# Kernel tuning notes

Hardware: AMD Instinct MI355X
Metric: run time of the kernel (lower is better)

## Reference

```python
import jax, jax.numpy as jnp
import numpy as np
from jax import lax

NUM_TAGS = 126
T = NUM_TAGS + 2          # tag_size = 128
B, S = 256, 512
START, STOP = T - 3, T - 2
NEG = -10000.0


def setup_inputs() -> dict:
    key = jax.random.key(0)
    k1, k2, k3 = jax.random.split(key, 3)
    feats = jax.random.normal(k1, (B, S, T), jnp.float32)
    # learned transition matrix with the module's init masking pattern
    trans = jax.random.normal(k2, (T, T), jnp.float32)
    trans = trans.at[:, START].set(NEG).at[STOP, :].set(NEG)
    trans = trans.at[:, 0].set(NEG).at[0, :].set(NEG)
    # prefix masks with varying valid lengths in [S/2, S]
    lengths = jax.random.randint(k3, (B,), S // 2, S + 1)
    mask = jnp.arange(S)[None, :] < lengths[:, None]
    return {"feats": feats, "mask": mask, "transitions": trans}


def reference(feats, mask, transitions):
    # Viterbi decode (module.forward returns (None, decode_idx)).
    Bn, Sn, Tn = feats.shape
    start, stop = Tn - 3, Tn - 2
    emit = jnp.transpose(feats, (1, 0, 2))            # (S, B, T)
    m = jnp.transpose(mask.astype(jnp.int32))         # (S, B)
    lengths = mask.astype(jnp.int32).sum(axis=1)      # (B,)

    part0 = emit[0] + transitions[start][None, :]     # (B, T)

    def step(part, inp):
        e_t, m_t = inp
        # scores[t, b, i, j] = feats[t, b, j] + transitions[i, j]
        cur = part[:, :, None] + transitions[None, :, :] + e_t[:, None, :]  # (B, from, to)
        new_part = cur.max(axis=1)                                          # (B, T)
        bp = jnp.argmax(cur, axis=1).astype(jnp.int32)                      # (B, T)
        bp = jnp.where(m_t[:, None] > 0, bp, 0)
        return new_part, (new_part, bp)

    _, (hist, bps) = lax.scan(step, part0, (emit[1:], m[1:]))
    part_hist = jnp.concatenate([part0[None], hist], axis=0)                # (S, B, T)
    back_points = jnp.concatenate(
        [bps, jnp.zeros((1, Bn, Tn), jnp.int32)], axis=0)                   # (S, B, T)

    bidx = jnp.arange(Bn)
    last_pos = lengths - 1                                                  # (B,)
    last_partition = part_hist[last_pos, bidx]                              # (B, T)
    last_bp = jnp.argmax(last_partition[:, :, None] + transitions[None], axis=1)
    pointer = last_bp[:, stop].astype(jnp.int32)                            # (B,)

    # overwrite back_points at the last valid position with the final pointer
    bp_bt = jnp.transpose(back_points, (1, 0, 2))                           # (B, S, T)
    bp_bt = bp_bt.at[bidx, last_pos].set(
        jnp.broadcast_to(pointer[:, None], (Bn, Tn)))
    back_points = jnp.transpose(bp_bt, (1, 0, 2))                           # (S, B, T)

    def trace(ptr, bp_t):
        new_ptr = jnp.take_along_axis(bp_t, ptr[:, None], axis=1)[:, 0]
        return new_ptr, new_ptr

    _, rev = lax.scan(trace, pointer, back_points[:-1], reverse=True)       # (S-1, B)
    decode = jnp.concatenate([rev, pointer[None]], axis=0)                  # (S, B)
    return jnp.transpose(decode)                                            # (B, S)
```

## Files before the change

kernel.cpp:

```cpp
#include <hip/hip_runtime.h>
#include <cstdint>
#include <cstddef>

constexpr int T_ = 128;
constexpr int S_ = 512;
constexpr int B_ = 256;
constexpr int START_ = T_ - 3;
constexpr int STOP_  = T_ - 2;
constexpr float NEGINF_ = -3.402823466e38f;

__device__ __forceinline__ void lds_barrier() {
  asm volatile("s_waitcnt lgkmcnt(0)\n\ts_barrier" ::: "memory");
}

__device__ __forceinline__ float readlane_f(float v, int sl) {
  return __int_as_float(__builtin_amdgcn_readlane(__float_as_int(v), sl));
}

__global__ __launch_bounds__(256) void viterbi_forward(
    const float* __restrict__ feats,
    const float* __restrict__ trans,
    float* __restrict__ ph)
{
  const int b   = blockIdx.x;
  const int tid = threadIdx.x;
  const int j   = tid >> 1;
  const int h   = tid & 1;

  __shared__ alignas(16) float part[2][T_];

  float tc[64];
  #pragma unroll
  for (int ii = 0; ii < 64; ++ii)
    tc[ii] = trans[(h * 64 + ii) * T_ + j];

  const float* fb = feats + (size_t)b * S_ * T_;

  float p0 = fb[j] + trans[START_ * T_ + j];
  if (h == 0) {
    part[0][j] = p0;
    ph[(size_t)b * T_ + j] = p0;
  }
  float e_next = fb[T_ + j];
  __syncthreads();

  for (int t = 1; t < S_; ++t) {
    float e_cur = e_next;
    if (t + 1 < S_) e_next = fb[(size_t)(t + 1) * T_ + j];

    const float4* p4 = (const float4*)part[(t - 1) & 1];
    float m0 = NEGINF_, m1 = NEGINF_, m2 = NEGINF_, m3 = NEGINF_;
    #pragma unroll
    for (int q = 0; q < 16; q += 4) {
      float4 a0 = p4[h * 16 + q + 0];
      float4 a1 = p4[h * 16 + q + 1];
      float4 a2 = p4[h * 16 + q + 2];
      float4 a3 = p4[h * 16 + q + 3];
      m0 = fmaxf(m0, fmaxf(fmaxf(a0.x + tc[4*q+ 0], a0.y + tc[4*q+ 1]),
                           fmaxf(a0.z + tc[4*q+ 2], a0.w + tc[4*q+ 3])));
      m1 = fmaxf(m1, fmaxf(fmaxf(a1.x + tc[4*q+ 4], a1.y + tc[4*q+ 5]),
                           fmaxf(a1.z + tc[4*q+ 6], a1.w + tc[4*q+ 7])));
      m2 = fmaxf(m2, fmaxf(fmaxf(a2.x + tc[4*q+ 8], a2.y + tc[4*q+ 9]),
                           fmaxf(a2.z + tc[4*q+10], a2.w + tc[4*q+11])));
      m3 = fmaxf(m3, fmaxf(fmaxf(a3.x + tc[4*q+12], a3.y + tc[4*q+13]),
                           fmaxf(a3.z + tc[4*q+14], a3.w + tc[4*q+15])));
    }
    float m = fmaxf(fmaxf(m0, m1), fmaxf(m2, m3));
    int sw = __builtin_amdgcn_mov_dpp(__float_as_int(m), 0xB1, 0xF, 0xF, true);
    m = fmaxf(m, __int_as_float(sw));
    float np = m + e_cur;
    if (h == 0) part[t & 1][j] = np;
    lds_barrier();
    if (h == 0) ph[((size_t)t * B_ + b) * T_ + j] = np;
  }
}

constexpr int CH_ = 8;
constexpr int TS_ = 130;

__global__ __launch_bounds__(64) void viterbi_trace(
    const float* __restrict__ feats,
    const void*  __restrict__ mask,
    const float* __restrict__ trans,
    const float* __restrict__ ph,
    int* __restrict__ out)
{
  const int b    = blockIdx.x;
  const int lane = threadIdx.x;

  __shared__ alignas(16) float transT[T_ * TS_];
  #pragma unroll 4
  for (int g = lane; g < T_ * T_; g += 64) {
    int i = g >> 7, jj = g & (T_ - 1);
    transT[jj * TS_ + i] = trans[g];
  }
  __syncthreads();

  int len = 0;
  {
    const int w0 = *(const int*)mask;
    if (w0 == 0x01010101) {
      const unsigned char* m = (const unsigned char*)mask + (size_t)b * S_;
      for (int s = lane; s < S_; s += 64) len += (m[s] != 0);
    } else if (w0 == 0x3F800000) {
      const float* m = (const float*)mask + (size_t)b * S_;
      for (int s = lane; s < S_; s += 64) len += (m[s] != 0.0f);
    } else {
      const int* m = (const int*)mask + (size_t)b * S_;
      for (int s = lane; s < S_; s += 64) len += (m[s] != 0);
    }
    #pragma unroll
    for (int o = 32; o > 0; o >>= 1) len += __shfl_xor(len, o);
  }
  const int lp = len - 1;

  const float2 L = *(const float2*)(ph + ((size_t)lp * B_ + b) * T_ + 2 * lane);
  float v0 = L.x + transT[STOP_ * TS_ + 2 * lane];
  float v1 = L.y + transT[STOP_ * TS_ + 2 * lane + 1];
  float mx = fmaxf(v0, v1);
  #pragma unroll
  for (int o = 32; o > 0; o >>= 1) mx = fmaxf(mx, __shfl_xor(mx, o));
  {
    unsigned long long g0 = __ballot(v0 == mx);
    unsigned long long g1 = __ballot(v1 == mx);
    int p0 = g0 ? 2 * (__ffsll(g0) - 1)     : (1 << 30);
    int p1 = g1 ? 2 * (__ffsll(g1) - 1) + 1 : (1 << 30);
    int pointer = min(p0, p1);

    for (int k = lp + 1 + lane; k <= S_ - 2; k += 64) out[b * S_ + k] = 0;
    if (lane == 0) {
      out[b * S_ + (S_ - 1)] = pointer;
      if (lp < S_ - 1) out[b * S_ + lp] = pointer;
    }

    int   ptr = pointer;
    float tg  = readlane_f((ptr & 1) ? L.y : L.x, ptr >> 1);
    const float* fb = feats + (size_t)b * S_ * T_;
    const float2 FL = *(const float2*)(fb + (size_t)lp * T_ + 2 * lane);
    float e = readlane_f((ptr & 1) ? FL.y : FL.x, ptr >> 1);

    float2 PA[CH_], FA[CH_], PB[CH_], FB[CH_];

    auto issue = [&](float2 (&P)[CH_], float2 (&F)[CH_], int k0) {
      #pragma unroll
      for (int s = 0; s < CH_; ++s) {
        int k = k0 - s; if (k < 0) k = 0;
        P[s] = *(const float2*)(ph + ((size_t)k * B_ + b) * T_ + 2 * lane);
        F[s] = *(const float2*)(fb + (size_t)k * T_ + 2 * lane);
      }
    };
    auto process = [&](const float2 (&P)[CH_], const float2 (&F)[CH_], int k0) {
      #pragma unroll
      for (int s = 0; s < CH_; ++s) {
        const int k = k0 - s;
        if (k >= 0) {
          const float2 tr = *(const float2*)(transT + ptr * TS_ + 2 * lane);
          float cx = (P[s].x + tr.x) + e;
          float cy = (P[s].y + tr.y) + e;
          unsigned long long q0 = __ballot(cx == tg);
          unsigned long long q1 = __ballot(cy == tg);
          int a0 = q0 ? 2 * (__ffsll(q0) - 1)     : (1 << 30);
          int a1 = q1 ? 2 * (__ffsll(q1) - 1) + 1 : (1 << 30);
          ptr = min(a0, a1);
          if (lane == 0) out[b * S_ + k] = ptr;
          tg = readlane_f((ptr & 1) ? P[s].y : P[s].x, ptr >> 1);
          e  = readlane_f((ptr & 1) ? F[s].y : F[s].x, ptr >> 1);
        }
      }
    };

    issue(PA, FA, lp - 1);
    for (int k0 = lp - 1; k0 >= 0; k0 -= 2 * CH_) {
      issue(PB, FB, k0 - CH_);
      process(PA, FA, k0);
      issue(PA, FA, k0 - 2 * CH_);
      process(PB, FB, k0 - CH_);
    }
  }
}

extern "C" void kernel_launch(void* const* d_in, const int* in_sizes, int n_in,
                              void* d_out, int out_size, void* d_ws, size_t ws_size,
                              hipStream_t stream) {
  const float* feats = (const float*)d_in[0];
  const void*  mask  = d_in[1];
  const float* trans = (const float*)d_in[2];
  float* ph = (float*)d_ws;
  int*   out = (int*)d_out;

  viterbi_forward<<<dim3(B_), dim3(256), 0, stream>>>(feats, trans, ph);
  viterbi_trace  <<<dim3(B_), dim3(64), 0, stream>>>(feats, mask, trans, ph, out);
}
```

Measured before the change: 465.2 us.

## Remap Viterbi forward threads to 4 outputs each with 8-lane DPP max reduction

```diff
diff --git a/kernel.cpp b/kernel.cpp
--- a/kernel.cpp
+++ b/kernel.cpp
@@ -17,61 +17,82 @@
   return __int_as_float(__builtin_amdgcn_readlane(__float_as_int(v), sl));
 }
 
+__device__ __forceinline__ float ig_reduce_max(float m) {
+  int x = __builtin_amdgcn_mov_dpp(__float_as_int(m), 0xB1, 0xF, 0xF, true);
+  m = fmaxf(m, __int_as_float(x));
+  x = __builtin_amdgcn_mov_dpp(__float_as_int(m), 0x4E, 0xF, 0xF, true);
+  m = fmaxf(m, __int_as_float(x));
+  x = __builtin_amdgcn_mov_dpp(__float_as_int(m), 0x141, 0xF, 0xF, true);
+  m = fmaxf(m, __int_as_float(x));
+  return m;
+}
+
 __global__ __launch_bounds__(256) void viterbi_forward(
     const float* __restrict__ feats,
     const float* __restrict__ trans,
     float* __restrict__ ph)
 {
-  const int b   = blockIdx.x;
-  const int tid = threadIdx.x;
-  const int j   = tid >> 1;
-  const int h   = tid & 1;
-
-  __shared__ alignas(16) float part[2][T_];
-
-  float tc[64];
+  const int tid  = threadIdx.x;
+  const int lane = tid & 63;
+  const int w    = tid >> 6;
+  const int ig   = lane & 7;
+  const int jl   = lane >> 3;
+  const int jg   = w * 8 + jl;
+  const int j0   = jg * 4;
+  const int b    = blockIdx.x;
+
+  __shared__ alignas(16) float part[2][160];
+
+  float4 tc[16];
   #pragma unroll
-  for (int ii = 0; ii < 64; ++ii)
-    tc[ii] = trans[(h * 64 + ii) * T_ + j];
+  for (int ii = 0; ii < 16; ++ii)
+    tc[ii] = *(const float4*)&trans[(16 * ig + ii) * T_ + j0];
 
   const float* fb = feats + (size_t)b * S_ * T_;
-
-  float p0 = fb[j] + trans[START_ * T_ + j];
-  if (h == 0) {
-    part[0][j] = p0;
-    ph[(size_t)b * T_ + j] = p0;
-  }
-  float e_next = fb[T_ + j];
+  const int woff = j0 + 4 * (jg >> 2);
+
+  float4 e0 = *(const float4*)&fb[j0];
+  float4 ts = *(const float4*)&trans[START_ * T_ + j0];
+  float4 p0 = make_float4(e0.x + ts.x, e0.y + ts.y, e0.z + ts.z, e0.w + ts.w);
+  if (ig == 0) {
+    *(float4*)&part[0][woff] = p0;
+    *(float4*)&ph[(size_t)b * T_ + j0] = p0;
+  }
+  float4 e_next = *(const float4*)&fb[T_ + j0];
   __syncthreads();
 
   for (int t = 1; t < S_; ++t) {
-    float e_cur = e_next;
-    if (t + 1 < S_) e_next = fb[(size_t)(t + 1) * T_ + j];
+    float4 e_cur = e_next;
+    if (t + 1 < S_) e_next = *(const float4*)&fb[(size_t)(t + 1) * T_ + j0];
 
     const float4* p4 = (const float4*)part[(t - 1) & 1];
+    float4 p[4];
+    #pragma unroll
+    for (int q = 0; q < 4; ++q) p[q] = p4[5 * ig + q];
+
     float m0 = NEGINF_, m1 = NEGINF_, m2 = NEGINF_, m3 = NEGINF_;
     #pragma unroll
-    for (int q = 0; q < 16; q += 4) {
-      float4 a0 = p4[h * 16 + q + 0];
-      float4 a1 = p4[h * 16 + q + 1];
-      float4 a2 = p4[h * 16 + q + 2];
-      float4 a3 = p4[h * 16 + q + 3];
-      m0 = fmaxf(m0, fmaxf(fmaxf(a0.x + tc[4*q+ 0], a0.y + tc[4*q+ 1]),
-                           fmaxf(a0.z + tc[4*q+ 2], a0.w + tc[4*q+ 3])));
-      m1 = fmaxf(m1, fmaxf(fmaxf(a1.x + tc[4*q+ 4], a1.y + tc[4*q+ 5]),
-                           fmaxf(a1.z + tc[4*q+ 6], a1.w + tc[4*q+ 7])));
-      m2 = fmaxf(m2, fmaxf(fmaxf(a2.x + tc[4*q+ 8], a2.y + tc[4*q+ 9]),
-                           fmaxf(a2.z + tc[4*q+10], a2.w + tc[4*q+11])));
-      m3 = fmaxf(m3, fmaxf(fmaxf(a3.x + tc[4*q+12], a3.y + tc[4*q+13]),
-                           fmaxf(a3.z + tc[4*q+14], a3.w + tc[4*q+15])));
-    }
-    float m = fmaxf(fmaxf(m0, m1), fmaxf(m2, m3));
-    int sw = __builtin_amdgcn_mov_dpp(__float_as_int(m), 0xB1, 0xF, 0xF, true);
-    m = fmaxf(m, __int_as_float(sw));
-    float np = m + e_cur;
-    if (h == 0) part[t & 1][j] = np;
+    for (int q = 0; q < 4; ++q) {
+      float4 pv = p[q];
+      float4 t0 = tc[4 * q + 0], t1 = tc[4 * q + 1];
+      float4 t2 = tc[4 * q + 2], t3 = tc[4 * q + 3];
+      m0 = fmaxf(m0, fmaxf(fmaxf(pv.x + t0.x, pv.y + t1.x),
+                           fmaxf(pv.z + t2.x, pv.w + t3.x)));
+      m1 = fmaxf(m1, fmaxf(fmaxf(pv.x + t0.y, pv.y + t1.y),
+                           fmaxf(pv.z + t2.y, pv.w + t3.y)));
+      m2 = fmaxf(m2, fmaxf(fmaxf(pv.x + t0.z, pv.y + t1.z),
+                           fmaxf(pv.z + t2.z, pv.w + t3.z)));
+      m3 = fmaxf(m3, fmaxf(fmaxf(pv.x + t0.w, pv.y + t1.w),
+                           fmaxf(pv.z + t2.w, pv.w + t3.w)));
+    }
+    float4 np4 = make_float4(ig_reduce_max(m0) + e_cur.x,
+                             ig_reduce_max(m1) + e_cur.y,
+                             ig_reduce_max(m2) + e_cur.z,
+                             ig_reduce_max(m3) + e_cur.w);
+    if (ig == 0) *(float4*)&part[t & 1][woff] = np4;
     lds_barrier();
-    if (h == 0) ph[((size_t)t * B_ + b) * T_ + j] = np;
+    if (ig == 0)
+      *(float4*)&ph[((size_t)t * B_ + b) * T_ + j0] = np4;
   }
 }
 
```

New measurement: 455.4 us. 1.02x faster.
